# Performance work log

Hardware: AMD Instinct MI355X
Metric: run time of the kernel (lower is better)

Reference implementation:

```python
import jax, jax.numpy as jnp
import numpy as np

B, S, D = 4, 2048, 1024
H = 16
HS = D // H  # 64


def setup_inputs() -> dict:
    key = jax.random.key(0)
    ks = jax.random.split(key, 6)
    scale = 1.0 / np.sqrt(D)
    x = jax.random.normal(ks[0], (B, S, D), dtype=jnp.float32)
    # per-head projection weights, stacked: [H, D, HS]
    Wq = jax.random.normal(ks[1], (H, D, HS), dtype=jnp.float32) * scale
    Wk = jax.random.normal(ks[2], (H, D, HS), dtype=jnp.float32) * scale
    Wv = jax.random.normal(ks[3], (H, D, HS), dtype=jnp.float32) * scale
    Wo = jax.random.normal(ks[4], (D, D), dtype=jnp.float32) * scale
    bo = jax.random.normal(ks[5], (D,), dtype=jnp.float32) * 0.01
    return {"x": x, "Wq": Wq, "Wk": Wk, "Wv": Wv, "Wo": Wo, "bo": bo}


def reference(x, Wq, Wk, Wv, Wo, bo):
    # Per-head dense projections (no bias): [B,S,D] x [H,D,HS] -> [B,H,S,HS]
    q = jnp.einsum('bsd,hde->bhse', x, Wq)
    k = jnp.einsum('bsd,hde->bhse', x, Wk)
    v = jnp.einsum('bsd,hde->bhse', x, Wv)
    # scaled dot-product scores: [B,H,S,S]
    scores = jnp.einsum('bhse,bhte->bhst', q, k) / jnp.sqrt(jnp.asarray(HS, dtype=x.dtype))
    # causal mask (lower triangular kept)
    causal = jnp.tril(jnp.ones((S, S), dtype=bool))
    scores = jnp.where(causal, scores, -jnp.inf)
    attn = jax.nn.softmax(scores, axis=-1)
    # dropout is identity at inference (rate handled as 0)
    out = jnp.einsum('bhst,bhte->bhse', attn, v)  # [B,H,S,HS]
    # concat heads: [B,S,H*HS] = [B,S,D]
    out = jnp.transpose(out, (0, 2, 1, 3)).reshape(B, S, D)
    return out @ Wo + bo
```

## Files before the change

kernel.cpp:

```cpp
#include <hip/hip_runtime.h>
#include <hip/hip_bf16.h>
#include <stdint.h>

#define NB 4
#define NS 2048
#define ND 1024
#define NH 16
#define NHS 64
#define NEG_BIG (-1e30f)
#define Q_SCALE 0.18033688011112042f

typedef __bf16 bf16x8 __attribute__((ext_vector_type(8)));
typedef float floatx4 __attribute__((ext_vector_type(4)));
typedef short s16x4 __attribute__((ext_vector_type(4)));

#if defined(__has_builtin)
#if __has_builtin(__builtin_amdgcn_mfma_f32_16x16x16bf16_1k)
#define HAVE_MFMA1K 1
#endif
#endif
#ifndef HAVE_MFMA1K
#define HAVE_MFMA1K 0
#endif

static constexpr size_t WSLAB = (size_t)NH * ND * NHS;
static constexpr size_t QSLAB = (size_t)NB * NH * NS * NHS;
static constexpr size_t XSLAB = (size_t)NB * NS * ND;

__device__ __forceinline__ uint16_t f2b(float f) {
    union { __hip_bfloat16 h; uint16_t u; } cv;
    cv.h = __float2bfloat16(f);
    return cv.u;
}

__device__ __forceinline__ void gll16(const void* g, void* l) {
  __builtin_amdgcn_global_load_lds(
      (__attribute__((address_space(1))) void*)(uintptr_t)g,
      (__attribute__((address_space(3))) void*)(uintptr_t)l,
      16, 0, 0);
}

__global__ __launch_bounds__(256) void k_prep(
    const float* __restrict__ x, const float* __restrict__ Wq,
    const float* __restrict__ Wk, const float* __restrict__ Wv,
    const float* __restrict__ Wo, uint16_t* __restrict__ xb,
    uint16_t* __restrict__ wt) {
  __shared__ __align__(16) uint16_t T[64][72];
  int bid = blockIdx.x;
  int tid = threadIdx.x;
  if (bid < 4096) {
    size_t i0 = ((size_t)bid * 256 + tid) * 8;
    float4 f0 = *(const float4*)&x[i0];
    float4 f1 = *(const float4*)&x[i0 + 4];
    __align__(16) uint16_t tmp[8];
    tmp[0] = f2b(f0.x); tmp[1] = f2b(f0.y); tmp[2] = f2b(f0.z); tmp[3] = f2b(f0.w);
    tmp[4] = f2b(f1.x); tmp[5] = f2b(f1.y); tmp[6] = f2b(f1.z); tmp[7] = f2b(f1.w);
    *(uint4*)&xb[i0] = *(uint4*)tmp;
    return;
  }
  bid -= 4096;
  const float* src; uint16_t* dst;
  int srcStride, dstStride, r0, c0;
  if (bid < 768) {
    int mat = bid >> 8;
    int rem = bid & 255;
    int h = rem >> 4, dt = rem & 15;
    const float* W = (mat == 0) ? Wq : (mat == 1) ? Wk : Wv;
    src = W + (size_t)h * (ND * NHS);
    dst = wt + (size_t)mat * WSLAB + (size_t)h * (NHS * ND);
    srcStride = NHS; dstStride = ND;
    r0 = dt * 64; c0 = 0;
  } else {
    int rem = bid - 768;
    int dt = rem >> 4, et = rem & 15;
    src = Wo; dst = wt + 3 * WSLAB;
    srcStride = ND; dstStride = ND;
    r0 = dt * 64; c0 = et * 64;
  }
  for (int u = tid; u < 1024; u += 256) {
    int row = u >> 4, cq = u & 15;
    float4 f = *(const float4*)&src[(size_t)(r0 + row) * srcStride + c0 + cq * 4];
    uint16_t* p = &T[row][cq * 4];
    p[0] = f2b(f.x); p[1] = f2b(f.y); p[2] = f2b(f.z); p[3] = f2b(f.w);
  }
  __syncthreads();
  for (int u = tid; u < 512; u += 256) {
    int c = u >> 3, cg = u & 7;
    __align__(16) uint16_t tmp[8];
    for (int j = 0; j < 8; j++) tmp[j] = T[cg * 8 + j][c];
    *(uint4*)&dst[(size_t)(c0 + c) * dstStride + r0 + cg * 8] = *(uint4*)tmp;
  }
}

__global__ __launch_bounds__(512, 4) void k_qkv(
    const uint16_t* __restrict__ xb, const uint16_t* __restrict__ wt,
    uint16_t* __restrict__ qk, uint16_t* __restrict__ vt) {
  __shared__ __align__(16) uint16_t L[32768];

  int bid = blockIdx.x;
  int xcd = bid & 7, idx = bid >> 3;
  int mtile = xcd * 8 + (idx & 7);
  int ntile = idx >> 3;
  int m0 = mtile * 128;
  int n0 = ntile * 128;

  int tid = threadIdx.x;
  int wave = tid >> 6, lane = tid & 63, quad = lane >> 4, l16 = lane & 15;
  int wr = wave >> 2, wc = wave & 3;

  int swc = ((tid & 3) ^ ((tid >> 4) & 3)) * 8;
  const uint16_t* pA = xb + (size_t)(m0 + (tid >> 2)) * ND + swc;
  const uint16_t* pB = wt + (size_t)(n0 + (tid >> 2)) * ND + swc;
  const int stOff = wave * 512;

  const int rq = (quad ^ (l16 >> 2)) * 8;
  const int offA = (wr * 64 + l16) * 32 + rq;
  const int offB = (wc * 32 + l16) * 32 + rq;

  floatx4 acc[4][2];
  #pragma unroll
  for (int i = 0; i < 4; i++)
    #pragma unroll
    for (int j = 0; j < 2; j++) acc[i][j] = (floatx4){0.f, 0.f, 0.f, 0.f};

#define STAGE(A_)                                                               \
  do {                                                                          \
    int a_ = (A_);                                                              \
    if (a_ < 32) {                                                              \
      int ko_ = (a_ >> 1) * 64 + (a_ & 1) * 32;                                 \
      gll16(pA + ko_, &L[(a_ & 3) * 4096 + stOff]);                             \
      gll16(pB + ko_, &L[16384 + (a_ & 3) * 4096 + stOff]);                     \
    }                                                                           \
  } while (0)

#define PH_BAR()                         \
  do {                                   \
    asm volatile("" ::: "memory");       \
    __builtin_amdgcn_s_barrier();        \
    asm volatile("" ::: "memory");       \
  } while (0)

  STAGE(0); STAGE(1); STAGE(2);
  asm volatile("s_waitcnt vmcnt(4)" ::: "memory");
  PH_BAR();

#define MFMA8()                                                                           \
  _Pragma("unroll")                                                                       \
  for (int mt_ = 0; mt_ < 4; mt_++)                                                       \
    _Pragma("unroll")                                                                     \
    for (int nt_ = 0; nt_ < 2; nt_++)                                                     \
      acc[mt_][nt_] = __builtin_amdgcn_mfma_f32_16x16x32_bf16(af[mt_], bfr[nt_], acc[mt_][nt_], 0, 0, 0)

  for (int t = 0; t < 16; ++t) {
    {
      int sA = ((2 * t) & 3) * 4096;
      int sB = 16384 + ((2 * t) & 3) * 4096;
      bf16x8 af[4], bfr[2];
      #pragma unroll
      for (int i = 0; i < 4; i++) af[i] = *(const bf16x8*)&L[sA + offA + i * 512];
      #pragma unroll
      for (int i = 0; i < 2; i++) bfr[i] = *(const bf16x8*)&L[sB + offB + i * 512];
      STAGE(2 * t + 3);
      PH_BAR();
      __builtin_amdgcn_s_setprio(1);
      MFMA8();
      __builtin_amdgcn_s_setprio(0);
      if (t < 15) { asm volatile("s_waitcnt vmcnt(4)" ::: "memory"); }
      else        { asm volatile("s_waitcnt vmcnt(0)" ::: "memory"); }
      PH_BAR();
    }
    {
      int sA = ((2 * t + 1) & 3) * 4096;
      int sB = 16384 + ((2 * t + 1) & 3) * 4096;
      bf16x8 af[4], bfr[2];
      #pragma unroll
      for (int i = 0; i < 4; i++) af[i] = *(const bf16x8*)&L[sA + offA + i * 512];
      #pragma unroll
      for (int i = 0; i < 2; i++) bfr[i] = *(const bf16x8*)&L[sB + offB + i * 512];
      STAGE(2 * t + 4);
      PH_BAR();
      __builtin_amdgcn_s_setprio(1);
      MFMA8();
      __builtin_amdgcn_s_setprio(0);
      if (t < 14)       { asm volatile("s_waitcnt vmcnt(4)" ::: "memory"); }
      else if (t == 14) { asm volatile("s_waitcnt vmcnt(2)" ::: "memory"); }
      if (t < 15) PH_BAR();
    }
  }
#undef MFMA8
#undef STAGE
#undef PH_BAR

  int matid = n0 >> 10;
  int b = m0 >> 11;
  if (matid == 2) {
    int hh = ((n0 - 2048) >> 6) + (wc >> 1);
    #pragma unroll
    for (int nt = 0; nt < 2; nt++) {
      int e = (wc & 1) * 32 + nt * 16 + l16;
      uint16_t* vrow = vt + ((size_t)(b * 16 + hh) * 64 + e) * NS;
      #pragma unroll
      for (int mt = 0; mt < 4; mt++) {
        __align__(8) uint16_t t4v[4];
        #pragma unroll
        for (int r = 0; r < 4; r++) t4v[r] = f2b(acc[mt][nt][r]);
        int s = (m0 & 2047) + wr * 64 + mt * 16 + quad * 4;
        *(uint2*)&vrow[s] = *(uint2*)t4v;
      }
    }
  } else {
    float scale = (matid == 0) ? Q_SCALE : 1.0f;
    uint16_t* base = qk + (size_t)matid * QSLAB;
    int hh = ((n0 & 1023) >> 6) + (wc >> 1);
    #pragma unroll
    for (int mt = 0; mt < 4; mt++) {
      int s = (m0 & 2047) + wr * 64 + mt * 16 + quad * 4;
      size_t rbase = ((size_t)(b * 16 + hh) * NS + s) * NHS;
      #pragma unroll
      for (int nt = 0; nt < 2; nt++)
        #pragma unroll
        for (int r = 0; r < 4; r++)
          base[rbase + (size_t)r * NHS + (wc & 1) * 32 + nt * 16 + l16] =
              f2b(acc[mt][nt][r] * scale);
    }
  }
}

#if HAVE_MFMA1K
__global__ __launch_bounds__(256, 4) void k_attn(
    const uint16_t* __restrict__ Q, const uint16_t* __restrict__ K,
    const uint16_t* __restrict__ VT, uint16_t* __restrict__ Y) {
  __shared__ __align__(16) uint16_t Ks[64][72];
  __shared__ __align__(16) uint16_t Vs[64][72];
  int bh = blockIdx.y;
  int b = bh >> 4, h = bh & 15;
  int ta = blockIdx.x;
  int tb = 31 - ta;
  const uint16_t* Qp = Q + (size_t)bh * (NS * NHS);
  const uint16_t* Kp = K + (size_t)bh * (NS * NHS);
  const uint16_t* Vp = VT + (size_t)bh * (NS * NHS);
  int tid = threadIdx.x;
  int wv = tid >> 6, lane = tid & 63, quad = lane >> 4, l16 = lane & 15;

  int row0 = tid >> 3, cg0 = tid & 7;
  int row1 = (tid + 256) >> 3, cg1 = tid & 7;

  int rA = ta * 64 + wv * 16 + l16;
  int rB = tb * 64 + wv * 16 + l16;
  bf16x8 aqA0 = *(const bf16x8*)&Qp[(size_t)rA * NHS + quad * 8];
  bf16x8 aqA1 = *(const bf16x8*)&Qp[(size_t)rA * NHS + 32 + quad * 8];
  bf16x8 aqB0 = *(const bf16x8*)&Qp[(size_t)rB * NHS + quad * 8];
  bf16x8 aqB1 = *(const bf16x8*)&Qp[(size_t)rB * NHS + 32 + quad * 8];

  float lAs = 0.f, lBs = 0.f;
  floatx4 oA[4], oB[4];
  for (int et = 0; et < 4; et++) {
    oA[et] = (floatx4){0.f, 0.f, 0.f, 0.f};
    oB[et] = (floatx4){0.f, 0.f, 0.f, 0.f};
  }

  uint4 rk0, rk1, rv0, rv1;
  rk0 = *(const uint4*)&Kp[(size_t)(0 * 64 + row0) * NHS + cg0 * 8];
  rk1 = *(const uint4*)&Kp[(size_t)(0 * 64 + row1) * NHS + cg1 * 8];
  rv0 = *(const uint4*)&Vp[(size_t)row0 * NS + 0 * 64 + cg0 * 8];
  rv1 = *(const uint4*)&Vp[(size_t)row1 * NS + 0 * 64 + cg1 * 8];

  for (int kt = 0; kt <= tb; kt++) {
    bool doA = (kt <= ta);
    __syncthreads();
    *(uint4*)&Ks[row0][cg0 * 8] = rk0;
    *(uint4*)&Ks[row1][cg1 * 8] = rk1;
    *(uint4*)&Vs[row0][cg0 * 8] = rv0;
    *(uint4*)&Vs[row1][cg1 * 8] = rv1;
    __syncthreads();
    if (kt < tb) {
      rk0 = *(const uint4*)&Kp[(size_t)((kt + 1) * 64 + row0) * NHS + cg0 * 8];
      rk1 = *(const uint4*)&Kp[(size_t)((kt + 1) * 64 + row1) * NHS + cg1 * 8];
      rv0 = *(const uint4*)&Vp[(size_t)row0 * NS + (kt + 1) * 64 + cg0 * 8];
      rv1 = *(const uint4*)&Vp[(size_t)row1 * NS + (kt + 1) * 64 + cg1 * 8];
    }

    s16x4 pbA[4], pbB[4];
    for (int ct = 0; ct < 4; ct++) {
      bf16x8 kb0 = *(const bf16x8*)&Ks[ct * 16 + l16][quad * 8];
      bf16x8 kb1 = *(const bf16x8*)&Ks[ct * 16 + l16][32 + quad * 8];
      int key = kt * 64 + ct * 16 + quad * 4;
      floatx4 c = (floatx4){0.f, 0.f, 0.f, 0.f};
      c = __builtin_amdgcn_mfma_f32_16x16x32_bf16(kb0, aqB0, c, 0, 0, 0);
      c = __builtin_amdgcn_mfma_f32_16x16x32_bf16(kb1, aqB1, c, 0, 0, 0);
      for (int r = 0; r < 4; r++) {
        float s = (kt == tb && key + r > rB) ? NEG_BIG : c[r];
        float p = __builtin_amdgcn_exp2f(s);
        lBs += p;
        pbB[ct][r] = (short)f2b(p);
      }
      if (doA) {
        floatx4 d = (floatx4){0.f, 0.f, 0.f, 0.f};
        d = __builtin_amdgcn_mfma_f32_16x16x32_bf16(kb0, aqA0, d, 0, 0, 0);
        d = __builtin_amdgcn_mfma_f32_16x16x32_bf16(kb1, aqA1, d, 0, 0, 0);
        for (int r = 0; r < 4; r++) {
          float s = (kt == ta && key + r > rA) ? NEG_BIG : d[r];
          float p = __builtin_amdgcn_exp2f(s);
          lAs += p;
          pbA[ct][r] = (short)f2b(p);
        }
      }
    }
    for (int et = 0; et < 4; et++)
      for (int ct = 0; ct < 4; ct++) {
        s16x4 va = *(const s16x4*)&Vs[et * 16 + l16][ct * 16 + quad * 4];
        oB[et] = __builtin_amdgcn_mfma_f32_16x16x16bf16_1k(va, pbB[ct], oB[et], 0, 0, 0);
        if (doA)
          oA[et] = __builtin_amdgcn_mfma_f32_16x16x16bf16_1k(va, pbA[ct], oA[et], 0, 0, 0);
      }
  }
  lAs += __shfl_xor(lAs, 16, 64); lAs += __shfl_xor(lAs, 32, 64);
  lBs += __shfl_xor(lBs, 16, 64); lBs += __shfl_xor(lBs, 32, 64);
  float invA = 1.f / lAs, invB = 1.f / lBs;
  uint16_t* yb = Y + (size_t)b * NS * ND + (size_t)h * NHS;
  for (int et = 0; et < 4; et++) {
    __align__(8) uint16_t tA[4], tB[4];
    for (int r = 0; r < 4; r++) {
      tA[r] = f2b(oA[et][r] * invA);
      tB[r] = f2b(oB[et][r] * invB);
    }
    *(uint2*)&yb[(size_t)rA * ND + et * 16 + quad * 4] = *(uint2*)tA;
    *(uint2*)&yb[(size_t)rB * ND + et * 16 + quad * 4] = *(uint2*)tB;
  }
}
#else
__global__ __launch_bounds__(256) void k_attn(
    const uint16_t* __restrict__ Q, const uint16_t* __restrict__ K,
    const uint16_t* __restrict__ VT, uint16_t* __restrict__ Y) {
  __shared__ __align__(16) uint16_t Ks[64][72];
  __shared__ __align__(16) uint16_t Vs[64][72];
  __shared__ __align__(16) uint16_t Ps[4][2][16][72];
  int bh = blockIdx.y;
  int b = bh >> 4, h = bh & 15;
  int ta = blockIdx.x;
  int tb = 31 - ta;
  const uint16_t* Qp = Q + (size_t)bh * (NS * NHS);
  const uint16_t* Kp = K + (size_t)bh * (NS * NHS);
  const uint16_t* Vp = VT + (size_t)bh * (NS * NHS);
  int tid = threadIdx.x;
  int wv = tid >> 6, lane = tid & 63, quad = lane >> 4, l16 = lane & 15;

  int rA = ta * 64 + wv * 16 + l16;
  int rB = tb * 64 + wv * 16 + l16;
  bf16x8 aqA0 = *(const bf16x8*)&Qp[(size_t)rA * NHS + quad * 8];
  bf16x8 aqA1 = *(const bf16x8*)&Qp[(size_t)rA * NHS + 32 + quad * 8];
  bf16x8 aqB0 = *(const bf16x8*)&Qp[(size_t)rB * NHS + quad * 8];
  bf16x8 aqB1 = *(const bf16x8*)&Qp[(size_t)rB * NHS + 32 + quad * 8];

  float lA[4] = {0.f, 0.f, 0.f, 0.f}, lB[4] = {0.f, 0.f, 0.f, 0.f};
  floatx4 oA[4], oB[4];
  for (int ct = 0; ct < 4; ct++) {
    oA[ct] = (floatx4){0.f, 0.f, 0.f, 0.f};
    oB[ct] = (floatx4){0.f, 0.f, 0.f, 0.f};
  }
  for (int kt = 0; kt <= tb; kt++) {
    bool doA = (kt <= ta);
    __syncthreads();
    for (int u = tid; u < 512; u += 256) {
      int row = u >> 3, cg = u & 7;
      *(uint4*)&Ks[row][cg * 8] =
          *(const uint4*)&Kp[(size_t)(kt * 64 + row) * NHS + cg * 8];
    }
    for (int u = tid; u < 512; u += 256) {
      int row = u >> 3, cg = u & 7;
      *(uint4*)&Vs[row][cg * 8] =
          *(const uint4*)&Vp[(size_t)row * NS + kt * 64 + cg * 8];
    }
    __syncthreads();
    floatx4 sA[4], sB[4];
    for (int ct = 0; ct < 4; ct++) {
      bf16x8 kb0 = *(const bf16x8*)&Ks[ct * 16 + l16][quad * 8];
      bf16x8 kb1 = *(const bf16x8*)&Ks[ct * 16 + l16][32 + quad * 8];
      floatx4 c = (floatx4){0.f, 0.f, 0.f, 0.f};
      c = __builtin_amdgcn_mfma_f32_16x16x32_bf16(aqB0, kb0, c, 0, 0, 0);
      c = __builtin_amdgcn_mfma_f32_16x16x32_bf16(aqB1, kb1, c, 0, 0, 0);
      sB[ct] = c;
      if (doA) {
        floatx4 d = (floatx4){0.f, 0.f, 0.f, 0.f};
        d = __builtin_amdgcn_mfma_f32_16x16x32_bf16(aqA0, kb0, d, 0, 0, 0);
        d = __builtin_amdgcn_mfma_f32_16x16x32_bf16(aqA1, kb1, d, 0, 0, 0);
        sA[ct] = d;
      }
    }
    if (kt == tb) {
      int qrb = tb * 64 + wv * 16 + quad * 4;
      for (int ct = 0; ct < 4; ct++) {
        int kg = kt * 64 + ct * 16 + l16;
        for (int r = 0; r < 4; r++)
          sB[ct][r] = (kg <= qrb + r) ? sB[ct][r] : NEG_BIG;
      }
    }
    if (doA && kt == ta) {
      int qrb = ta * 64 + wv * 16 + quad * 4;
      for (int ct = 0; ct < 4; ct++) {
        int kg = kt * 64 + ct * 16 + l16;
        for (int r = 0; r < 4; r++)
          sA[ct][r] = (kg <= qrb + r) ? sA[ct][r] : NEG_BIG;
      }
    }
    for (int ct = 0; ct < 4; ct++)
      for (int r = 0; r < 4; r++) {
        float p = __builtin_amdgcn_exp2f(sB[ct][r]);
        lB[r] += p;
        Ps[wv][1][quad * 4 + r][ct * 16 + l16] = f2b(p);
      }
    if (doA)
      for (int ct = 0; ct < 4; ct++)
        for (int r = 0; r < 4; r++) {
          float p = __builtin_amdgcn_exp2f(sA[ct][r]);
          lA[r] += p;
          Ps[wv][0][quad * 4 + r][ct * 16 + l16] = f2b(p);
        }
    bf16x8 apB0 = *(const bf16x8*)&Ps[wv][1][l16][quad * 8];
    bf16x8 apB1 = *(const bf16x8*)&Ps[wv][1][l16][32 + quad * 8];
    bf16x8 apA0, apA1;
    if (doA) {
      apA0 = *(const bf16x8*)&Ps[wv][0][l16][quad * 8];
      apA1 = *(const bf16x8*)&Ps[wv][0][l16][32 + quad * 8];
    }
    for (int ct = 0; ct < 4; ct++) {
      bf16x8 vb0 = *(const bf16x8*)&Vs[ct * 16 + l16][quad * 8];
      bf16x8 vb1 = *(const bf16x8*)&Vs[ct * 16 + l16][32 + quad * 8];
      oB[ct] = __builtin_amdgcn_mfma_f32_16x16x32_bf16(apB0, vb0, oB[ct], 0, 0, 0);
      oB[ct] = __builtin_amdgcn_mfma_f32_16x16x32_bf16(apB1, vb1, oB[ct], 0, 0, 0);
      if (doA) {
        oA[ct] = __builtin_amdgcn_mfma_f32_16x16x32_bf16(apA0, vb0, oA[ct], 0, 0, 0);
        oA[ct] = __builtin_amdgcn_mfma_f32_16x16x32_bf16(apA1, vb1, oA[ct], 0, 0, 0);
      }
    }
  }
  for (int off = 1; off < 16; off <<= 1)
    for (int r = 0; r < 4; r++) {
      lA[r] += __shfl_xor(lA[r], off, 64);
      lB[r] += __shfl_xor(lB[r], off, 64);
    }
  uint16_t* yb = Y + (size_t)b * NS * ND + (size_t)h * NHS;
  for (int ct = 0; ct < 4; ct++)
    for (int r = 0; r < 4; r++) {
      int sA_ = ta * 64 + wv * 16 + quad * 4 + r;
      int sB_ = tb * 64 + wv * 16 + quad * 4 + r;
      yb[(size_t)sA_ * ND + ct * 16 + l16] = f2b(oA[ct][r] / lA[r]);
      yb[(size_t)sB_ * ND + ct * 16 + l16] = f2b(oB[ct][r] / lB[r]);
    }
}
#endif

__global__ __launch_bounds__(256) void k_proj(
    const uint16_t* __restrict__ y, const uint16_t* __restrict__ wot,
    const float* __restrict__ bo, float* __restrict__ out) {
  __shared__ __align__(16) uint16_t As[128 * 64];
  __shared__ __align__(16) uint16_t Bs[128 * 64];
  int m0 = blockIdx.x * 128;
  int n0 = blockIdx.y * 128;
  int tid = threadIdx.x;
  int wv = tid >> 6, lane = tid & 63, quad = lane >> 4, l16 = lane & 15;
  int wr = wv >> 1, wc = wv & 1;
  int srow = lane >> 3, scol = lane & 7;

  floatx4 acc[4][4];
  for (int i = 0; i < 4; i++)
    for (int j = 0; j < 4; j++) acc[i][j] = (floatx4){0.f, 0.f, 0.f, 0.f};

  for (int k0 = 0; k0 < ND; k0 += 64) {
    __syncthreads();
    for (int j = 0; j < 4; j++) {
      int rg = wv * 4 + j;
      int r = rg * 8 + srow;
      gll16(&y[(size_t)(m0 + r) * ND + k0 + scol * 8], &As[rg * 512]);
      gll16(&wot[(size_t)(n0 + r) * ND + k0 + scol * 8], &Bs[rg * 512]);
    }
    __syncthreads();
    for (int kk = 0; kk < 2; kk++) {
      bf16x8 af[4], bfr[4];
      for (int t = 0; t < 4; t++) {
        af[t]  = *(const bf16x8*)&As[(wr * 64 + t * 16 + l16) * 64 + kk * 32 + quad * 8];
        bfr[t] = *(const bf16x8*)&Bs[(wc * 64 + t * 16 + l16) * 64 + kk * 32 + quad * 8];
      }
      for (int mt = 0; mt < 4; mt++)
        for (int nt = 0; nt < 4; nt++)
          acc[mt][nt] = __builtin_amdgcn_mfma_f32_16x16x32_bf16(af[mt], bfr[nt], acc[mt][nt], 0, 0, 0);
    }
  }
  for (int mt = 0; mt < 4; mt++)
    for (int nt = 0; nt < 4; nt++)
      for (int r = 0; r < 4; r++) {
        int s = m0 + wr * 64 + mt * 16 + quad * 4 + r;
        int n = n0 + wc * 64 + nt * 16 + l16;
        out[(size_t)s * ND + n] = acc[mt][nt][r] + bo[n];
      }
}

extern "C" void kernel_launch(void* const* d_in, const int* in_sizes, int n_in,
                              void* d_out, int out_size, void* d_ws, size_t ws_size,
                              hipStream_t stream) {
  const float* x  = (const float*)d_in[0];
  const float* Wq = (const float*)d_in[1];
  const float* Wk = (const float*)d_in[2];
  const float* Wv = (const float*)d_in[3];
  const float* Wo = (const float*)d_in[4];
  const float* bo = (const float*)d_in[5];
  uint16_t* ws = (uint16_t*)d_ws;

  uint16_t* wt = ws;
  uint16_t* xb = ws + 4 * WSLAB;
  uint16_t* q  = xb + XSLAB;
  uint16_t* k  = q + QSLAB;
  uint16_t* vt = k + QSLAB;
  uint16_t* y  = vt + QSLAB;

  k_prep<<<dim3(5120), dim3(256), 0, stream>>>(x, Wq, Wk, Wv, Wo, xb, wt);
  k_qkv<<<dim3(1536), dim3(512), 0, stream>>>(xb, wt, q, vt);
  k_attn<<<dim3(16, NB * NH), dim3(256), 0, stream>>>(q, k, vt, y);
  k_proj<<<dim3(64, 8), dim3(256), 0, stream>>>(y, wt + 3 * WSLAB, bo, (float*)d_out);
}
```

Baseline: 253.2 us.

## Double-buffer K/V tiles in attention and remap block order for cache locality

```diff
diff --git a/kernel.cpp b/kernel.cpp
--- a/kernel.cpp
+++ b/kernel.cpp
@@ -230,12 +230,13 @@
 __global__ __launch_bounds__(256, 4) void k_attn(
     const uint16_t* __restrict__ Q, const uint16_t* __restrict__ K,
     const uint16_t* __restrict__ VT, uint16_t* __restrict__ Y) {
-  __shared__ __align__(16) uint16_t Ks[64][72];
-  __shared__ __align__(16) uint16_t Vs[64][72];
-  int bh = blockIdx.y;
+  __shared__ __align__(16) uint16_t Ks[2][64][72];
+  __shared__ __align__(16) uint16_t Vs[2][64][72];
+  int bid = blockIdx.x;
+  int ta = (bid >> 3) & 15;
+  int tb = 31 - ta;
+  int bh = (bid & 7) + (bid >> 7) * 8;
   int b = bh >> 4, h = bh & 15;
-  int ta = blockIdx.x;
-  int tb = 31 - ta;
   const uint16_t* Qp = Q + (size_t)bh * (NS * NHS);
   const uint16_t* Kp = K + (size_t)bh * (NS * NHS);
   const uint16_t* Vp = VT + (size_t)bh * (NS * NHS);
@@ -243,7 +244,7 @@
   int wv = tid >> 6, lane = tid & 63, quad = lane >> 4, l16 = lane & 15;
 
   int row0 = tid >> 3, cg0 = tid & 7;
-  int row1 = (tid + 256) >> 3, cg1 = tid & 7;
+  int row1 = row0 + 32;
 
   int rA = ta * 64 + wv * 16 + l16;
   int rB = tb * 64 + wv * 16 + l16;
@@ -260,34 +261,46 @@
   }
 
   uint4 rk0, rk1, rv0, rv1;
-  rk0 = *(const uint4*)&Kp[(size_t)(0 * 64 + row0) * NHS + cg0 * 8];
-  rk1 = *(const uint4*)&Kp[(size_t)(0 * 64 + row1) * NHS + cg1 * 8];
-  rv0 = *(const uint4*)&Vp[(size_t)row0 * NS + 0 * 64 + cg0 * 8];
-  rv1 = *(const uint4*)&Vp[(size_t)row1 * NS + 0 * 64 + cg1 * 8];
+  rk0 = *(const uint4*)&Kp[(size_t)row0 * NHS + cg0 * 8];
+  rk1 = *(const uint4*)&Kp[(size_t)row1 * NHS + cg0 * 8];
+  rv0 = *(const uint4*)&Vp[(size_t)row0 * NS + cg0 * 8];
+  rv1 = *(const uint4*)&Vp[(size_t)row1 * NS + cg0 * 8];
+  *(uint4*)&Ks[0][row0][cg0 * 8] = rk0;
+  *(uint4*)&Ks[0][row1][cg0 * 8] = rk1;
+  *(uint4*)&Vs[0][row0][cg0 * 8] = rv0;
+  *(uint4*)&Vs[0][row1][cg0 * 8] = rv1;
+  rk0 = *(const uint4*)&Kp[(size_t)(64 + row0) * NHS + cg0 * 8];
+  rk1 = *(const uint4*)&Kp[(size_t)(64 + row1) * NHS + cg0 * 8];
+  rv0 = *(const uint4*)&Vp[(size_t)row0 * NS + 64 + cg0 * 8];
+  rv1 = *(const uint4*)&Vp[(size_t)row1 * NS + 64 + cg0 * 8];
+  __syncthreads();
 
   for (int kt = 0; kt <= tb; kt++) {
+    int cur = kt & 1;
+    if (kt < tb) {
+      *(uint4*)&Ks[cur ^ 1][row0][cg0 * 8] = rk0;
+      *(uint4*)&Ks[cur ^ 1][row1][cg0 * 8] = rk1;
+      *(uint4*)&Vs[cur ^ 1][row0][cg0 * 8] = rv0;
+      *(uint4*)&Vs[cur ^ 1][row1][cg0 * 8] = rv1;
+      if (kt + 2 <= tb) {
+        rk0 = *(const uint4*)&Kp[(size_t)((kt + 2) * 64 + row0) * NHS + cg0 * 8];
+        rk1 = *(const uint4*)&Kp[(size_t)((kt + 2) * 64 + row1) * NHS + cg0 * 8];
+        rv0 = *(const uint4*)&Vp[(size_t)row0 * NS + (kt + 2) * 64 + cg0 * 8];
+        rv1 = *(const uint4*)&Vp[(size_t)row1 * NS + (kt + 2) * 64 + cg0 * 8];
+      }
+    }
     bool doA = (kt <= ta);
-    __syncthreads();
-    *(uint4*)&Ks[row0][cg0 * 8] = rk0;
-    *(uint4*)&Ks[row1][cg1 * 8] = rk1;
-    *(uint4*)&Vs[row0][cg0 * 8] = rv0;
-    *(uint4*)&Vs[row1][cg1 * 8] = rv1;
-    __syncthreads();
-    if (kt < tb) {
-      rk0 = *(const uint4*)&Kp[(size_t)((kt + 1) * 64 + row0) * NHS + cg0 * 8];
-      rk1 = *(const uint4*)&Kp[(size_t)((kt + 1) * 64 + row1) * NHS + cg1 * 8];
-      rv0 = *(const uint4*)&Vp[(size_t)row0 * NS + (kt + 1) * 64 + cg0 * 8];
-      rv1 = *(const uint4*)&Vp[(size_t)row1 * NS + (kt + 1) * 64 + cg1 * 8];
-    }
 
     s16x4 pbA[4], pbB[4];
+    #pragma unroll
     for (int ct = 0; ct < 4; ct++) {
-      bf16x8 kb0 = *(const bf16x8*)&Ks[ct * 16 + l16][quad * 8];
-      bf16x8 kb1 = *(const bf16x8*)&Ks[ct * 16 + l16][32 + quad * 8];
+      bf16x8 kb0 = *(const bf16x8*)&Ks[cur][ct * 16 + l16][quad * 8];
+      bf16x8 kb1 = *(const bf16x8*)&Ks[cur][ct * 16 + l16][32 + quad * 8];
       int key = kt * 64 + ct * 16 + quad * 4;
       floatx4 c = (floatx4){0.f, 0.f, 0.f, 0.f};
       c = __builtin_amdgcn_mfma_f32_16x16x32_bf16(kb0, aqB0, c, 0, 0, 0);
       c = __builtin_amdgcn_mfma_f32_16x16x32_bf16(kb1, aqB1, c, 0, 0, 0);
+      #pragma unroll
       for (int r = 0; r < 4; r++) {
         float s = (kt == tb && key + r > rB) ? NEG_BIG : c[r];
         float p = __builtin_amdgcn_exp2f(s);
@@ -298,6 +311,7 @@
         floatx4 d = (floatx4){0.f, 0.f, 0.f, 0.f};
         d = __builtin_amdgcn_mfma_f32_16x16x32_bf16(kb0, aqA0, d, 0, 0, 0);
         d = __builtin_amdgcn_mfma_f32_16x16x32_bf16(kb1, aqA1, d, 0, 0, 0);
+        #pragma unroll
         for (int r = 0; r < 4; r++) {
           float s = (kt == ta && key + r > rA) ? NEG_BIG : d[r];
           float p = __builtin_amdgcn_exp2f(s);
@@ -306,14 +320,18 @@
         }
       }
     }
+    #pragma unroll
     for (int et = 0; et < 4; et++)
+      #pragma unroll
       for (int ct = 0; ct < 4; ct++) {
-        s16x4 va = *(const s16x4*)&Vs[et * 16 + l16][ct * 16 + quad * 4];
+        s16x4 va = *(const s16x4*)&Vs[cur][et * 16 + l16][ct * 16 + quad * 4];
         oB[et] = __builtin_amdgcn_mfma_f32_16x16x16bf16_1k(va, pbB[ct], oB[et], 0, 0, 0);
         if (doA)
           oA[et] = __builtin_amdgcn_mfma_f32_16x16x16bf16_1k(va, pbA[ct], oA[et], 0, 0, 0);
       }
-  }
+    __syncthreads();
+  }
+
   lAs += __shfl_xor(lAs, 16, 64); lAs += __shfl_xor(lAs, 32, 64);
   lBs += __shfl_xor(lBs, 16, 64); lBs += __shfl_xor(lBs, 32, 64);
   float invA = 1.f / lAs, invB = 1.f / lBs;
@@ -335,10 +353,11 @@
   __shared__ __align__(16) uint16_t Ks[64][72];
   __shared__ __align__(16) uint16_t Vs[64][72];
   __shared__ __align__(16) uint16_t Ps[4][2][16][72];
-  int bh = blockIdx.y;
+  int bid = blockIdx.x;
+  int ta = (bid >> 3) & 15;
+  int tb = 31 - ta;
+  int bh = (bid & 7) + (bid >> 7) * 8;
   int b = bh >> 4, h = bh & 15;
-  int ta = blockIdx.x;
-  int tb = 31 - ta;
   const uint16_t* Qp = Q + (size_t)bh * (NS * NHS);
   const uint16_t* Kp = K + (size_t)bh * (NS * NHS);
   const uint16_t* Vp = VT + (size_t)bh * (NS * NHS);
@@ -515,6 +534,6 @@
 
   k_prep<<<dim3(5120), dim3(256), 0, stream>>>(x, Wq, Wk, Wv, Wo, xb, wt);
   k_qkv<<<dim3(1536), dim3(512), 0, stream>>>(xb, wt, q, vt);
-  k_attn<<<dim3(16, NB * NH), dim3(256), 0, stream>>>(q, k, vt, y);
+  k_attn<<<dim3(1024), dim3(256), 0, stream>>>(q, k, vt, y);
   k_proj<<<dim3(64, 8), dim3(256), 0, stream>>>(y, wt + 3 * WSLAB, bo, (float*)d_out);
 }
```

New measurement: 449.0 us. +77.3%, slower.

## Rewrite output projection GEMM with 4-stage LDS pipeline and XCD-aware tile mapping

Applied to the files above, without the earlier changes.

```diff
diff --git a/kernel.cpp b/kernel.cpp
--- a/kernel.cpp
+++ b/kernel.cpp
@@ -450,49 +450,119 @@
 }
 #endif
 
-__global__ __launch_bounds__(256) void k_proj(
+__global__ __launch_bounds__(512, 4) void k_proj(
     const uint16_t* __restrict__ y, const uint16_t* __restrict__ wot,
     const float* __restrict__ bo, float* __restrict__ out) {
-  __shared__ __align__(16) uint16_t As[128 * 64];
-  __shared__ __align__(16) uint16_t Bs[128 * 64];
-  int m0 = blockIdx.x * 128;
-  int n0 = blockIdx.y * 128;
+  __shared__ __align__(16) uint16_t L[32768];
+
+  int bid = blockIdx.x;
+  int xcd = bid & 7, idx = bid >> 3;
+  int mtile = xcd * 8 + (idx & 7);
+  int ntile = idx >> 3;
+  int m0 = mtile * 128;
+  int n0 = ntile * 128;
+
   int tid = threadIdx.x;
-  int wv = tid >> 6, lane = tid & 63, quad = lane >> 4, l16 = lane & 15;
-  int wr = wv >> 1, wc = wv & 1;
-  int srow = lane >> 3, scol = lane & 7;
-
-  floatx4 acc[4][4];
+  int wave = tid >> 6, lane = tid & 63, quad = lane >> 4, l16 = lane & 15;
+  int wr = wave >> 2, wc = wave & 3;
+
+  int swc = ((tid & 3) ^ ((tid >> 4) & 3)) * 8;
+  const uint16_t* pA = y + (size_t)(m0 + (tid >> 2)) * ND + swc;
+  const uint16_t* pB = wot + (size_t)(n0 + (tid >> 2)) * ND + swc;
+  const int stOff = wave * 512;
+
+  const int rq = (quad ^ (l16 >> 2)) * 8;
+  const int offA = (wr * 64 + l16) * 32 + rq;
+  const int offB = (wc * 32 + l16) * 32 + rq;
+
+  floatx4 acc[4][2];
+  #pragma unroll
   for (int i = 0; i < 4; i++)
-    for (int j = 0; j < 4; j++) acc[i][j] = (floatx4){0.f, 0.f, 0.f, 0.f};
-
-  for (int k0 = 0; k0 < ND; k0 += 64) {
-    __syncthreads();
-    for (int j = 0; j < 4; j++) {
-      int rg = wv * 4 + j;
-      int r = rg * 8 + srow;
-      gll16(&y[(size_t)(m0 + r) * ND + k0 + scol * 8], &As[rg * 512]);
-      gll16(&wot[(size_t)(n0 + r) * ND + k0 + scol * 8], &Bs[rg * 512]);
-    }
-    __syncthreads();
-    for (int kk = 0; kk < 2; kk++) {
-      bf16x8 af[4], bfr[4];
-      for (int t = 0; t < 4; t++) {
-        af[t]  = *(const bf16x8*)&As[(wr * 64 + t * 16 + l16) * 64 + kk * 32 + quad * 8];
-        bfr[t] = *(const bf16x8*)&Bs[(wc * 64 + t * 16 + l16) * 64 + kk * 32 + quad * 8];
-      }
-      for (int mt = 0; mt < 4; mt++)
-        for (int nt = 0; nt < 4; nt++)
-          acc[mt][nt] = __builtin_amdgcn_mfma_f32_16x16x32_bf16(af[mt], bfr[nt], acc[mt][nt], 0, 0, 0);
-    }
-  }
-  for (int mt = 0; mt < 4; mt++)
-    for (int nt = 0; nt < 4; nt++)
-      for (int r = 0; r < 4; r++) {
-        int s = m0 + wr * 64 + mt * 16 + quad * 4 + r;
-        int n = n0 + wc * 64 + nt * 16 + l16;
-        out[(size_t)s * ND + n] = acc[mt][nt][r] + bo[n];
-      }
+    #pragma unroll
+    for (int j = 0; j < 2; j++) acc[i][j] = (floatx4){0.f, 0.f, 0.f, 0.f};
+
+#define STAGE(A_)                                                               \
+  do {                                                                          \
+    int a_ = (A_);                                                              \
+    if (a_ < 32) {                                                              \
+      int ko_ = (a_ >> 1) * 64 + (a_ & 1) * 32;                                 \
+      gll16(pA + ko_, &L[(a_ & 3) * 4096 + stOff]);                             \
+      gll16(pB + ko_, &L[16384 + (a_ & 3) * 4096 + stOff]);                     \
+    }                                                                           \
+  } while (0)
+
+#define PH_BAR()                         \
+  do {                                   \
+    asm volatile("" ::: "memory");       \
+    __builtin_amdgcn_s_barrier();        \
+    asm volatile("" ::: "memory");       \
+  } while (0)
+
+  STAGE(0); STAGE(1); STAGE(2);
+  asm volatile("s_waitcnt vmcnt(4)" ::: "memory");
+  PH_BAR();
+
+#define MFMA8()                                                                           \
+  _Pragma("unroll")                                                                       \
+  for (int mt_ = 0; mt_ < 4; mt_++)                                                       \
+    _Pragma("unroll")                                                                     \
+    for (int nt_ = 0; nt_ < 2; nt_++)                                                     \
+      acc[mt_][nt_] = __builtin_amdgcn_mfma_f32_16x16x32_bf16(af[mt_], bfr[nt_], acc[mt_][nt_], 0, 0, 0)
+
+  for (int t = 0; t < 16; ++t) {
+    {
+      int sA = ((2 * t) & 3) * 4096;
+      int sB = 16384 + ((2 * t) & 3) * 4096;
+      bf16x8 af[4], bfr[2];
+      #pragma unroll
+      for (int i = 0; i < 4; i++) af[i] = *(const bf16x8*)&L[sA + offA + i * 512];
+      #pragma unroll
+      for (int i = 0; i < 2; i++) bfr[i] = *(const bf16x8*)&L[sB + offB + i * 512];
+      STAGE(2 * t + 3);
+      PH_BAR();
+      __builtin_amdgcn_s_setprio(1);
+      MFMA8();
+      __builtin_amdgcn_s_setprio(0);
+      if (t < 15) { asm volatile("s_waitcnt vmcnt(4)" ::: "memory"); }
+      else        { asm volatile("s_waitcnt vmcnt(0)" ::: "memory"); }
+      PH_BAR();
+    }
+    {
+      int sA = ((2 * t + 1) & 3) * 4096;
+      int sB = 16384 + ((2 * t + 1) & 3) * 4096;
+      bf16x8 af[4], bfr[2];
+      #pragma unroll
+      for (int i = 0; i < 4; i++) af[i] = *(const bf16x8*)&L[sA + offA + i * 512];
+      #pragma unroll
+      for (int i = 0; i < 2; i++) bfr[i] = *(const bf16x8*)&L[sB + offB + i * 512];
+      STAGE(2 * t + 4);
+      PH_BAR();
+      __builtin_amdgcn_s_setprio(1);
+      MFMA8();
+      __builtin_amdgcn_s_setprio(0);
+      if (t < 14)       { asm volatile("s_waitcnt vmcnt(4)" ::: "memory"); }
+      else if (t == 14) { asm volatile("s_waitcnt vmcnt(2)" ::: "memory"); }
+      if (t < 15) PH_BAR();
+    }
+  }
+#undef MFMA8
+#undef STAGE
+#undef PH_BAR
+
+  float bv[2];
+  #pragma unroll
+  for (int nt = 0; nt < 2; nt++) bv[nt] = bo[n0 + wc * 32 + nt * 16 + l16];
+  #pragma unroll
+  for (int mt = 0; mt < 4; mt++) {
+    int s = m0 + wr * 64 + mt * 16 + quad * 4;
+    #pragma unroll
+    for (int nt = 0; nt < 2; nt++) {
+      int n = n0 + wc * 32 + nt * 16 + l16;
+      #pragma unroll
+      for (int r = 0; r < 4; r++)
+        out[(size_t)(s + r) * ND + n] = acc[mt][nt][r] + bv[nt];
+    }
+  }
 }
 
 extern "C" void kernel_launch(void* const* d_in, const int* in_sizes, int n_in,
@@ -516,5 +586,5 @@
   k_prep<<<dim3(5120), dim3(256), 0, stream>>>(x, Wq, Wk, Wv, Wo, xb, wt);
   k_qkv<<<dim3(1536), dim3(512), 0, stream>>>(xb, wt, q, vt);
   k_attn<<<dim3(16, NB * NH), dim3(256), 0, stream>>>(q, k, vt, y);
-  k_proj<<<dim3(64, 8), dim3(256), 0, stream>>>(y, wt + 3 * WSLAB, bo, (float*)d_out);
-}
+  k_proj<<<dim3(512), dim3(512), 0, stream>>>(y, wt + 3 * WSLAB, bo, (float*)d_out);
+}
```

After: 253.7 us. Within noise of the previous version (+0.2%).
